# Kernel optimization log

Hardware: AMD Instinct MI355X
Metric: run time of the kernel (lower is better)

The kernel has to match this reference:

```python
import jax, jax.numpy as jnp
import numpy as np

N = 50000      # nodes
E = 800000     # directed edges (avg degree 16)
F_IN = 128     # dataset.num_features
H = 256        # hidden_channels
C = 40         # dataset.num_classes


def _glorot(k, shape):
    lim = float(np.sqrt(6.0 / (shape[0] + shape[1])))
    return jax.random.uniform(k, shape, jnp.float32, -lim, lim)


def setup_inputs() -> dict:
    key = jax.random.key(0)
    ks = jax.random.split(key, 8)
    x = jax.random.normal(ks[0], (N, F_IN), jnp.float32)
    edge_index = jax.random.randint(ks[1], (2, E), 0, N, dtype=jnp.int32)
    W1 = _glorot(ks[2], (F_IN, H));      b1 = jnp.zeros((H,), jnp.float32)
    W2 = _glorot(ks[3], (H, H // 2));    b2 = jnp.zeros((H // 2,), jnp.float32)
    W3 = _glorot(ks[4], (H // 2, H // 4)); b3 = jnp.zeros((H // 4,), jnp.float32)
    W4 = _glorot(ks[5], (H // 4, C));    b4 = jnp.zeros((C,), jnp.float32)
    return {"x": x, "edge_index": edge_index,
            "W1": W1, "b1": b1, "W2": W2, "b2": b2,
            "W3": W3, "b3": b3, "W4": W4, "b4": b4}


def reference(x, edge_index, W1, b1, W2, b2, W3, b3, W4, b4):
    # GCNConv with default add_self_loops=True and symmetric normalization.
    loops = jnp.arange(N, dtype=edge_index.dtype)
    src = jnp.concatenate([edge_index[0], loops])   # message sources
    dst = jnp.concatenate([edge_index[1], loops])   # aggregation targets
    # degree computed on target index (PyG default), incl. self-loops
    deg = jax.ops.segment_sum(jnp.ones_like(dst, jnp.float32), dst, num_segments=N)
    dinv = jnp.where(deg > 0, jax.lax.rsqrt(deg), 0.0)
    norm = dinv[src] * dinv[dst]                    # [E+N]

    def conv(h, W, b):
        h = h @ W                                   # transform first (PyG order)
        msg = h[src] * norm[:, None]                # gather + scale
        return jax.ops.segment_sum(msg, dst, num_segments=N) + b

    h = jax.nn.relu(conv(x, W1, b1))   # dropout = identity in eval mode
    h = jax.nn.relu(conv(h, W2, b2))
    h = jax.nn.relu(conv(h, W3, b3))
    return conv(h, W4, b4)
```

## Files before the change

kernel.cpp:

```cpp
#include <hip/hip_runtime.h>
#include <stdint.h>

#define NNODES 50000
#define NEDGES 800000
#define SCAN_NBLK ((NNODES + 255) / 256)
#define NB ((NNODES + 255) / 256)
#define EPB 4096
#define SCAT_NBLK ((NEDGES + EPB - 1) / EPB)

typedef __attribute__((ext_vector_type(8))) short bf16x8;
typedef __attribute__((ext_vector_type(4))) float f32x4;

__device__ inline unsigned short f2bf(float f) {
    unsigned u = __float_as_uint(f);
    return (unsigned short)((u + 0x7fffu + ((u >> 16) & 1u)) >> 16);
}
__device__ inline float bf2f(unsigned short h) {
    return __uint_as_float(((unsigned)h) << 16);
}


__global__ void zero_kernel(int* __restrict__ p, int n) {
    int i = blockIdx.x * blockDim.x + threadIdx.x;
    if (i < n) p[i] = 0;
}

__global__ __launch_bounds__(256) void bucket_count_kernel(const int* __restrict__ dst,
                                                           int* __restrict__ bhist) {
    __shared__ int h[NB];
    for (int b = threadIdx.x; b < NB; b += 256) h[b] = 0;
    __syncthreads();
    const int base = blockIdx.x * EPB;
#pragma unroll
    for (int i = 0; i < EPB / 256; ++i) {
        const int e = base + threadIdx.x + i * 256;
        if (e < NEDGES) atomicAdd(&h[dst[e] >> 8], 1);
    }
    __syncthreads();
    for (int b = threadIdx.x; b < NB; b += 256)
        if (h[b]) atomicAdd(&bhist[b], h[b]);
}

__global__ __launch_bounds__(256) void bucket_scan_kernel(const int* __restrict__ bhist,
                                                          int* __restrict__ bofs,
                                                          int* __restrict__ gcur) {
    __shared__ int s[256];
    const int t = threadIdx.x;
    s[t] = (t < NB) ? bhist[t] : 0;
    __syncthreads();
    for (int off = 1; off < 256; off <<= 1) {
        int v = (t >= off) ? s[t - off] : 0;
        __syncthreads();
        s[t] += v;
        __syncthreads();
    }
    if (t < NB) {
        const int excl = (t > 0) ? s[t - 1] : 0;
        bofs[t] = excl;
        gcur[t] = excl;
    }
    if (t == 255) bofs[NB] = s[255];
}

__global__ __launch_bounds__(256) void bucket_scatter_kernel(const int* __restrict__ src,
                                                             const int* __restrict__ dst,
                                                             int* __restrict__ gcur,
                                                             int2* __restrict__ gpair) {
    __shared__ int h[256];
    __shared__ int s[256];
    __shared__ int gof[256];
    __shared__ int2 pr[EPB];
    __shared__ int ga[EPB];

    const int t = threadIdx.x;
    const int base = blockIdx.x * EPB;
    const int nval = min(EPB, NEDGES - base);

    h[t] = 0;
    __syncthreads();
#pragma unroll
    for (int i = 0; i < EPB / 256; ++i) {
        const int e = base + t + i * 256;
        if (e < NEDGES) atomicAdd(&h[dst[e] >> 8], 1);
    }
    __syncthreads();
    s[t] = h[t];
    __syncthreads();
    for (int off = 1; off < 256; off <<= 1) {
        int v = (t >= off) ? s[t - off] : 0;
        __syncthreads();
        s[t] += v;
        __syncthreads();
    }
    {
        const int c = h[t];
        if (t < NB && c > 0) gof[t] = atomicAdd(&gcur[t], c);
        const int lofs = s[t] - c;
        h[t] = lofs;
        s[t] = lofs;
    }
    __syncthreads();
#pragma unroll
    for (int i = 0; i < EPB / 256; ++i) {
        const int e = base + t + i * 256;
        if (e < NEDGES) {
            const int d = dst[e];
            const int b = d >> 8;
            const int slot = atomicAdd(&h[b], 1);
            pr[slot] = make_int2(src[e], d);
            ga[slot] = gof[b] + (slot - s[b]);
        }
    }
    __syncthreads();
#pragma unroll
    for (int i = 0; i < EPB / 256; ++i) {
        const int slot = t + i * 256;
        if (slot < nval) gpair[ga[slot]] = pr[slot];
    }
}

__global__ __launch_bounds__(256) void deg_count_kernel(const int2* __restrict__ gpair,
                                                        const int* __restrict__ bofs,
                                                        int* __restrict__ cnt) {
    __shared__ int c[256];
    const int t = threadIdx.x;
    c[t] = 0;
    __syncthreads();
    const int beg = bofs[blockIdx.x], end = bofs[blockIdx.x + 1];
    for (int e = beg + t; e < end; e += 256) atomicAdd(&c[gpair[e].y & 255], 1);
    __syncthreads();
    const int node = blockIdx.x * 256 + t;
    if (node < NNODES) cnt[node] = c[t];
}

__global__ __launch_bounds__(256) void bucket_fill_kernel(const int2* __restrict__ gpair,
                                                          const int* __restrict__ bofs,
                                                          const int* __restrict__ rp,
                                                          int* __restrict__ col) {
    __shared__ int c[256];
    const int t = threadIdx.x;
    c[t] = 0;
    __syncthreads();
    const int beg = bofs[blockIdx.x], end = bofs[blockIdx.x + 1];
    for (int e = beg + t; e < end; e += 256) {
        const int2 p = gpair[e];
        const int r = atomicAdd(&c[p.y & 255], 1);
        col[rp[p.y] + r] = p.x;
    }
}


__global__ __launch_bounds__(256) void scan1_kernel(const int* __restrict__ cnt,
                                                    int* __restrict__ bsum) {
    const int i = blockIdx.x * 256 + threadIdx.x;
    int v = (i < NNODES) ? cnt[i] : 0;
#pragma unroll
    for (int off = 32; off > 0; off >>= 1) v += __shfl_down(v, off, 64);
    __shared__ int wsum[4];
    if ((threadIdx.x & 63) == 0) wsum[threadIdx.x >> 6] = v;
    __syncthreads();
    if (threadIdx.x == 0) bsum[blockIdx.x] = wsum[0] + wsum[1] + wsum[2] + wsum[3];
}

__global__ __launch_bounds__(256) void scan2_kernel(const int* __restrict__ bsum,
                                                    int* __restrict__ boff,
                                                    int* __restrict__ rp_last) {
    __shared__ int s[256];
    const int t = threadIdx.x;
    s[t] = (t < SCAN_NBLK) ? bsum[t] : 0;
    __syncthreads();
    for (int off = 1; off < 256; off <<= 1) {
        int v = (t >= off) ? s[t - off] : 0;
        __syncthreads();
        s[t] += v;
        __syncthreads();
    }
    if (t < SCAN_NBLK) boff[t] = (t > 0) ? s[t - 1] : 0;
    if (t == 255) rp_last[0] = s[255];
}

__global__ __launch_bounds__(256) void scan3_kernel(const int* __restrict__ cnt,
                                                    const int* __restrict__ boff,
                                                    int* __restrict__ rp,
                                                    float* __restrict__ dinv) {
    __shared__ int s[256];
    const int t = threadIdx.x;
    const int i = blockIdx.x * 256 + t;
    const int c = (i < NNODES) ? cnt[i] : 0;
    s[t] = c;
    __syncthreads();
    for (int off = 1; off < 256; off <<= 1) {
        int v = (t >= off) ? s[t - off] : 0;
        __syncthreads();
        s[t] += v;
        __syncthreads();
    }
    if (i < NNODES) {
        rp[i] = boff[blockIdx.x] + s[t] - c;
        dinv[i] = rsqrtf((float)(c + 1));
    }
}


__global__ __launch_bounds__(256) void cvt_kernel(const float* __restrict__ in,
                                                  unsigned short* __restrict__ out, int n4) {
    int i = blockIdx.x * 256 + threadIdx.x;
    if (i >= n4) return;
    float4 v = *(const float4*)(in + (size_t)i * 4);
    ushort4 h;
    h.x = f2bf(v.x); h.y = f2bf(v.y); h.z = f2bf(v.z); h.w = f2bf(v.w);
    *(ushort4*)(out + (size_t)i * 4) = h;
}


template <int VEC>
__device__ inline void vloadf(float (&d)[VEC], const float* __restrict__ p) {
    if constexpr (VEC == 2) { float2 t = *(const float2*)p; d[0]=t.x; d[1]=t.y; }
    else { d[0] = *p; }
}
template <int VEC>
__device__ inline void vloadbf(float (&d)[VEC], const unsigned short* __restrict__ p) {
    if constexpr (VEC == 2) {
        unsigned v = *(const unsigned*)p;
        d[0] = bf2f((unsigned short)(v & 0xffffu));
        d[1] = bf2f((unsigned short)(v >> 16));
    } else {
        d[0] = bf2f(*p);
    }
}
template <int VEC>
__device__ inline void vstoref(float* __restrict__ p, const float (&d)[VEC]) {
    if constexpr (VEC == 2) { *(float2*)p = make_float2(d[0], d[1]); }
    else { *p = d[0]; }
}

template <int F, int VEC, bool RELU, bool HAS_BIAS>
__global__ __launch_bounds__(256) void agg_kernel(const float* __restrict__ in32,
                                                  const unsigned short* __restrict__ inbf,
                                                  float* __restrict__ out,
                                                  const int* __restrict__ rp,
                                                  const int* __restrict__ colidx,
                                                  const float* __restrict__ dinv,
                                                  const float* __restrict__ bias) {
    const int wave = threadIdx.x >> 6;
    const int lane = threadIdx.x & 63;
    const int d = blockIdx.x * 4 + wave;
    if (d >= NNODES) return;
    constexpr int LANES = F / VEC;
    if (lane >= LANES) return;
    const int off = lane * VEC;

    const float dv = dinv[d];
    float acc[VEC];
    vloadf<VEC>(acc, in32 + (size_t)d * F + off);
#pragma unroll
    for (int v = 0; v < VEC; ++v) acc[v] *= dv;

    int j = rp[d];
    const int end = rp[d + 1];
    for (; j + 4 <= end; j += 4) {
        const int c0 = colidx[j + 0], c1 = colidx[j + 1], c2 = colidx[j + 2], c3 = colidx[j + 3];
        const float w0 = dinv[c0], w1 = dinv[c1], w2 = dinv[c2], w3 = dinv[c3];
        float t0[VEC], t1[VEC], t2[VEC], t3[VEC];
        vloadbf<VEC>(t0, inbf + (size_t)c0 * F + off);
        vloadbf<VEC>(t1, inbf + (size_t)c1 * F + off);
        vloadbf<VEC>(t2, inbf + (size_t)c2 * F + off);
        vloadbf<VEC>(t3, inbf + (size_t)c3 * F + off);
#pragma unroll
        for (int v = 0; v < VEC; ++v) acc[v] += w0 * t0[v] + w1 * t1[v] + w2 * t2[v] + w3 * t3[v];
    }
    for (; j < end; ++j) {
        const int c = colidx[j];
        const float wc = dinv[c];
        float t[VEC];
        vloadbf<VEC>(t, inbf + (size_t)c * F + off);
#pragma unroll
        for (int v = 0; v < VEC; ++v) acc[v] += wc * t[v];
    }

    float res[VEC];
#pragma unroll
    for (int v = 0; v < VEC; ++v) {
        float r = dv * acc[v];
        if constexpr (HAS_BIAS) r += bias[off + v];
        if constexpr (RELU) r = fmaxf(r, 0.0f);
        res[v] = r;
    }
    vstoref<VEC>(out + (size_t)d * F + off, res);
}


template <int K, int M>
__global__ __launch_bounds__(256) void repack_kernel(const float* __restrict__ W,
                                                     unsigned short* __restrict__ hi,
                                                     unsigned short* __restrict__ lo) {
    int i = blockIdx.x * 256 + threadIdx.x;
    if (i >= K * M) return;
    const int k = i / M, n = i % M;
    constexpr int KS = K / 32;
    const int cb = n >> 7;
    const int ct = (n >> 4) & 7;
    const int ln = ((k >> 3) & 3) * 16 + (n & 15);
    const int j  = k & 7;
    const int ks = k >> 5;
    const size_t o = ((((size_t)cb * KS + ks) * 8 + ct) * 64 + ln) * 8 + j;
    const float f = W[i];
    const unsigned short h = f2bf(f);
    hi[o] = h;
    lo[o] = f2bf(f - bf2f(h));
}


template <int K, int M, bool BIAS_RELU, bool WRITE_BF>
__global__ __launch_bounds__(256) void mfma_gemm_kernel(const float* __restrict__ A,
                                                        const unsigned short* __restrict__ Whi,
                                                        const unsigned short* __restrict__ Wlo,
                                                        const float* __restrict__ bias,
                                                        float* __restrict__ C,
                                                        unsigned short* __restrict__ Cbf) {
    constexpr int KS = K / 32;
    __shared__ char lds[32768];
    char* Ahi = lds;
    char* Alo = lds + 8192;
    char* Bhi = lds + 16384;
    char* Blo = lds + 24576;

    const int t = threadIdx.x;
    const int lane = t & 63;
    const int w = t >> 6;
    const int wr = w >> 1, wc = w & 1;
    const int r0 = blockIdx.x * 128;
    const int n0 = blockIdx.y * 128;

    const unsigned short* bhg = Whi + (size_t)blockIdx.y * KS * 4096;
    const unsigned short* blg = Wlo + (size_t)blockIdx.y * KS * 4096;

    f32x4 acc[4][4];
#pragma unroll
    for (int i = 0; i < 4; ++i)
#pragma unroll
        for (int j = 0; j < 4; ++j) acc[i][j] = (f32x4){0.f, 0.f, 0.f, 0.f};

    for (int ks = 0; ks < KS; ++ks) {
        const int k0 = ks * 32;

        {
            const char* gh = (const char*)(bhg + (size_t)ks * 4096);
            const char* gl = (const char*)(blg + (size_t)ks * 4096);
#pragma unroll
            for (int c = 0; c < 2; ++c) {
                const int ct = w * 2 + c;
                __builtin_amdgcn_global_load_lds(
                    (const __attribute__((address_space(1))) void*)(gh + ct * 1024 + lane * 16),
                    (__attribute__((address_space(3))) void*)(Bhi + ct * 1024), 16, 0, 0);
                __builtin_amdgcn_global_load_lds(
                    (const __attribute__((address_space(1))) void*)(gl + ct * 1024 + lane * 16),
                    (__attribute__((address_space(3))) void*)(Blo + ct * 1024), 16, 0, 0);
            }
        }

        float4 av[4];
#pragma unroll
        for (int i = 0; i < 4; ++i) {
            const int q = t + i * 256;
            const int row = q >> 3;
            const int kq = (q & 7) * 4;
            const int gr = r0 + row;
            float4 v = make_float4(0.f, 0.f, 0.f, 0.f);
            if (gr < NNODES) v = *(const float4*)(A + (size_t)gr * K + k0 + kq);
            av[i] = v;
        }
#pragma unroll
        for (int i = 0; i < 4; ++i) {
            const int q = t + i * 256;
            const int row = q >> 3;
            const int kq = (q & 7) * 4;
            const int rt = row >> 4, m = row & 15, quad = kq >> 3, j0 = kq & 7;
            const int off = rt * 1024 + (quad * 16 + m) * 16 + j0 * 2;
            const float4 v = av[i];
            ushort4 h, l;
            h.x = f2bf(v.x); l.x = f2bf(v.x - bf2f(h.x));
            h.y = f2bf(v.y); l.y = f2bf(v.y - bf2f(h.y));
            h.z = f2bf(v.z); l.z = f2bf(v.z - bf2f(h.z));
            h.w = f2bf(v.w); l.w = f2bf(v.w - bf2f(h.w));
            *(ushort4*)(Ahi + off) = h;
            *(ushort4*)(Alo + off) = l;
        }
        __syncthreads();

        bf16x8 ah[4], al[4], bh[4], bl[4];
#pragma unroll
        for (int i = 0; i < 4; ++i) {
            ah[i] = *(const bf16x8*)(Ahi + (wr * 4 + i) * 1024 + lane * 16);
            al[i] = *(const bf16x8*)(Alo + (wr * 4 + i) * 1024 + lane * 16);
            bh[i] = *(const bf16x8*)(Bhi + (wc * 4 + i) * 1024 + lane * 16);
            bl[i] = *(const bf16x8*)(Blo + (wc * 4 + i) * 1024 + lane * 16);
        }
#pragma unroll
        for (int i = 0; i < 4; ++i)
#pragma unroll
            for (int j = 0; j < 4; ++j) {
                acc[i][j] = __builtin_amdgcn_mfma_f32_16x16x32_bf16(ah[i], bh[j], acc[i][j], 0, 0, 0);
                acc[i][j] = __builtin_amdgcn_mfma_f32_16x16x32_bf16(ah[i], bl[j], acc[i][j], 0, 0, 0);
                acc[i][j] = __builtin_amdgcn_mfma_f32_16x16x32_bf16(al[i], bh[j], acc[i][j], 0, 0, 0);
            }
        __syncthreads();
    }

    const int quad = lane >> 4;
    const int cl = lane & 15;
#pragma unroll
    for (int i = 0; i < 4; ++i) {
#pragma unroll
        for (int j = 0; j < 4; ++j) {
            const int colg = n0 + wc * 64 + j * 16 + cl;
            float bv = 0.f;
            if constexpr (BIAS_RELU) bv = bias[colg];
#pragma unroll
            for (int r = 0; r < 4; ++r) {
                const int rowg = r0 + wr * 64 + i * 16 + quad * 4 + r;
                if (rowg < NNODES) {
                    float v = acc[i][j][r] + bv;
                    if constexpr (BIAS_RELU) v = fmaxf(v, 0.f);
                    C[(size_t)rowg * M + colg] = v;
                    if constexpr (WRITE_BF) Cbf[(size_t)rowg * M + colg] = f2bf(v);
                }
            }
        }
    }
}


template <int BM, int BN, int BK, int TM, int TN, bool BIAS_RELU, bool WRITE_BF>
__global__ __launch_bounds__(256) void gemm_kernel(const float* __restrict__ A,
                                                   const float* __restrict__ W,
                                                   const float* __restrict__ bias,
                                                   float* __restrict__ C,
                                                   unsigned short* __restrict__ Cbf,
                                                   int Nrows, int K, int M) {
    constexpr int TX = BN / TN;
    constexpr int TY = BM / TM;
    static_assert(TX * TY == 256, "thread grid must be 256");
    constexpr int A_LOADS = (BM * BK) / (256 * 4);
    constexpr int W_LOADS = (BN * BK) / (256 * 4);
    static_assert(A_LOADS >= 1 && W_LOADS >= 1, "tile too small");

    const int tid = threadIdx.x;
    const int tx = tid % TX;
    const int ty = tid / TX;
    const int r0 = blockIdx.x * BM;
    const int c0 = blockIdx.y * BN;

    __shared__ float As[BK][BM + 4];
    __shared__ float Ws[BK][BN];

    float acc[TM][TN] = {};

    for (int k0 = 0; k0 < K; k0 += BK) {
#pragma unroll
        for (int l = 0; l < A_LOADS; ++l) {
            const int idx = tid + l * 256;
            const int row = idx / (BK / 4);
            const int kq = idx % (BK / 4);
            float4 v = make_float4(0.f, 0.f, 0.f, 0.f);
            const int gr = r0 + row;
            if (gr < Nrows) v = *(const float4*)(A + (size_t)gr * K + k0 + kq * 4);
            As[kq * 4 + 0][row] = v.x;
            As[kq * 4 + 1][row] = v.y;
            As[kq * 4 + 2][row] = v.z;
            As[kq * 4 + 3][row] = v.w;
        }
#pragma unroll
        for (int l = 0; l < W_LOADS; ++l) {
            const int idx = tid + l * 256;
            const int kk = idx / (BN / 4);
            const int cq = idx % (BN / 4);
            const int gc = c0 + cq * 4;
            float4 v;
            const float* wrow = W + (size_t)(k0 + kk) * M;
            if (gc + 3 < M) {
                v = *(const float4*)(wrow + gc);
            } else {
                v.x = (gc + 0 < M) ? wrow[gc + 0] : 0.f;
                v.y = (gc + 1 < M) ? wrow[gc + 1] : 0.f;
                v.z = (gc + 2 < M) ? wrow[gc + 2] : 0.f;
                v.w = (gc + 3 < M) ? wrow[gc + 3] : 0.f;
            }
            *(float4*)&Ws[kk][cq * 4] = v;
        }
        __syncthreads();

#pragma unroll
        for (int kk = 0; kk < BK; ++kk) {
            float a[TM], b[TN];
#pragma unroll
            for (int i = 0; i < TM; ++i) a[i] = As[kk][ty * TM + i];
#pragma unroll
            for (int j = 0; j < TN; ++j) b[j] = Ws[kk][tx * TN + j];
#pragma unroll
            for (int i = 0; i < TM; ++i)
#pragma unroll
                for (int j = 0; j < TN; ++j) acc[i][j] += a[i] * b[j];
        }
        __syncthreads();
    }

#pragma unroll
    for (int i = 0; i < TM; ++i) {
        const int gr = r0 + ty * TM + i;
        if (gr >= Nrows) continue;
#pragma unroll
        for (int j = 0; j < TN; ++j) {
            const int gc = c0 + tx * TN + j;
            if (gc >= M) continue;
            float v = acc[i][j];
            if constexpr (BIAS_RELU) v = fmaxf(v + bias[gc], 0.0f);
            C[(size_t)gr * M + gc] = v;
            if constexpr (WRITE_BF) Cbf[(size_t)gr * M + gc] = f2bf(v);
        }
    }
}


extern "C" void kernel_launch(void* const* d_in, const int* in_sizes, int n_in,
                              void* d_out, int out_size, void* d_ws, size_t ws_size,
                              hipStream_t stream) {
    const float* x  = (const float*)d_in[0];
    const int* ei   = (const int*)d_in[1];
    const float* W1 = (const float*)d_in[2];
    const float* b1 = (const float*)d_in[3];
    const float* W2 = (const float*)d_in[4];
    const float* b2 = (const float*)d_in[5];
    const float* W3 = (const float*)d_in[6];
    const float* b3 = (const float*)d_in[7];
    const float* W4 = (const float*)d_in[8];
    const float* b4 = (const float*)d_in[9];
    float* out = (float*)d_out;
    const int* esrc = ei;
    const int* edst = ei + NEDGES;

    char* w = (char*)d_ws;
    auto alloc = [&](size_t bytes) -> void* {
        void* p = (void*)w;
        w += (bytes + 255) & ~(size_t)255;
        return p;
    };
    int* cnt    = (int*)alloc((size_t)NNODES * 4);
    int* rp     = (int*)alloc((size_t)(NNODES + 1) * 4);
    int* col    = (int*)alloc((size_t)NEDGES * 4);
    float* dinv = (float*)alloc((size_t)NNODES * 4);
    int* bsum   = (int*)alloc((size_t)SCAN_NBLK * 4);
    int* boff   = (int*)alloc((size_t)SCAN_NBLK * 4);
    int* bhist  = (int*)alloc((size_t)NB * 4);
    int* bofs   = (int*)alloc((size_t)(NB + 1) * 4);
    int* gcur   = (int*)alloc((size_t)NB * 4);
    int2* gpair = (int2*)alloc((size_t)NEDGES * 8);
    unsigned short* W1hi = (unsigned short*)alloc((size_t)128 * 256 * 2);
    unsigned short* W1lo = (unsigned short*)alloc((size_t)128 * 256 * 2);
    unsigned short* W2hi = (unsigned short*)alloc((size_t)256 * 128 * 2);
    unsigned short* W2lo = (unsigned short*)alloc((size_t)256 * 128 * 2);
    float* B0   = (float*)alloc((size_t)NNODES * 256 * 4);
    float* B1   = (float*)alloc((size_t)NNODES * 128 * 4);
    float* B2   = (float*)alloc((size_t)NNODES * 128 * 4);
    unsigned short* xbf  = (unsigned short*)alloc((size_t)NNODES * 128 * 2);
    unsigned short* B1bf = (unsigned short*)alloc((size_t)NNODES * 128 * 2);
    unsigned short* B0bf = (unsigned short*)alloc((size_t)NNODES * 64 * 2);

    repack_kernel<128, 256><<<(128 * 256 + 255) / 256, 256, 0, stream>>>(W1, W1hi, W1lo);
    repack_kernel<256, 128><<<(256 * 128 + 255) / 256, 256, 0, stream>>>(W2, W2hi, W2lo);
    cvt_kernel<<<(NNODES * 128 / 4 + 255) / 256, 256, 0, stream>>>(x, xbf, NNODES * 128 / 4);

    zero_kernel<<<1, 256, 0, stream>>>(bhist, NB);
    bucket_count_kernel<<<SCAT_NBLK, 256, 0, stream>>>(edst, bhist);
    bucket_scan_kernel<<<1, 256, 0, stream>>>(bhist, bofs, gcur);
    bucket_scatter_kernel<<<SCAT_NBLK, 256, 0, stream>>>(esrc, edst, gcur, gpair);
    deg_count_kernel<<<NB, 256, 0, stream>>>(gpair, bofs, cnt);
    scan1_kernel<<<SCAN_NBLK, 256, 0, stream>>>(cnt, bsum);
    scan2_kernel<<<1, 256, 0, stream>>>(bsum, boff, rp + NNODES);
    scan3_kernel<<<SCAN_NBLK, 256, 0, stream>>>(cnt, boff, rp, dinv);
    bucket_fill_kernel<<<NB, 256, 0, stream>>>(gpair, bofs, rp, col);

    const int aggGrid = (NNODES + 3) / 4;
    const int rowBlks = (NNODES + 127) / 128;

    agg_kernel<128, 2, false, false><<<aggGrid, 256, 0, stream>>>(x, xbf, B2, rp, col, dinv, nullptr);
    mfma_gemm_kernel<128, 256, true, false>
        <<<dim3(rowBlks, 2), 256, 0, stream>>>(B2, W1hi, W1lo, b1, B0, nullptr);

    mfma_gemm_kernel<256, 128, false, true>
        <<<dim3(rowBlks, 1), 256, 0, stream>>>(B0, W2hi, W2lo, nullptr, B1, B1bf);
    agg_kernel<128, 2, true, true><<<aggGrid, 256, 0, stream>>>(B1, B1bf, B2, rp, col, dinv, b2);

    gemm_kernel<64, 64, 16, 4, 4, false, true>
        <<<dim3((NNODES + 63) / 64, 1), 256, 0, stream>>>(B2, W3, nullptr, B0, B0bf, NNODES, 128, 64);
    agg_kernel<64, 1, true, true><<<aggGrid, 256, 0, stream>>>(B0, B0bf, B1, rp, col, dinv, b3);

    gemm_kernel<64, 64, 16, 4, 4, false, true>
        <<<dim3((NNODES + 63) / 64, 1), 256, 0, stream>>>(B1, W4, nullptr, B0, B0bf, NNODES, 64, 40);
    agg_kernel<40, 1, false, true><<<aggGrid, 256, 0, stream>>>(B0, B0bf, out, rp, col, dinv, b4);
}
```

Baseline: 383.7 us.

## Fuse CSR build into one per-bucket kernel and shrink MFMA GEMM row tile

Result: faster. 365.9 us (-4.6%).

```diff
diff --git a/kernel.cpp b/kernel.cpp
--- a/kernel.cpp
+++ b/kernel.cpp
@@ -3,7 +3,6 @@
 
 #define NNODES 50000
 #define NEDGES 800000
-#define SCAN_NBLK ((NNODES + 255) / 256)
 #define NB ((NNODES + 255) / 256)
 #define EPB 4096
 #define SCAT_NBLK ((NEDGES + EPB - 1) / EPB)
@@ -43,7 +42,8 @@
 
 __global__ __launch_bounds__(256) void bucket_scan_kernel(const int* __restrict__ bhist,
                                                           int* __restrict__ bofs,
-                                                          int* __restrict__ gcur) {
+                                                          int* __restrict__ gcur,
+                                                          int* __restrict__ rp_last) {
     __shared__ int s[256];
     const int t = threadIdx.x;
     s[t] = (t < NB) ? bhist[t] : 0;
@@ -59,17 +59,17 @@
         bofs[t] = excl;
         gcur[t] = excl;
     }
-    if (t == 255) bofs[NB] = s[255];
+    if (t == 255) { bofs[NB] = s[255]; rp_last[0] = s[255]; }
 }
 
 __global__ __launch_bounds__(256) void bucket_scatter_kernel(const int* __restrict__ src,
                                                              const int* __restrict__ dst,
                                                              int* __restrict__ gcur,
-                                                             int2* __restrict__ gpair) {
+                                                             unsigned* __restrict__ gpk) {
     __shared__ int h[256];
     __shared__ int s[256];
     __shared__ int gof[256];
-    __shared__ int2 pr[EPB];
+    __shared__ unsigned pr[EPB];
     __shared__ int ga[EPB];
 
     const int t = threadIdx.x;
@@ -107,7 +107,7 @@
             const int d = dst[e];
             const int b = d >> 8;
             const int slot = atomicAdd(&h[b], 1);
-            pr[slot] = make_int2(src[e], d);
+            pr[slot] = ((unsigned)(d & 255) << 16) | (unsigned)src[e];
             ga[slot] = gof[b] + (slot - s[b]);
         }
     }
@@ -115,59 +115,26 @@
 #pragma unroll
     for (int i = 0; i < EPB / 256; ++i) {
         const int slot = t + i * 256;
-        if (slot < nval) gpair[ga[slot]] = pr[slot];
-    }
-}
-
-__global__ __launch_bounds__(256) void deg_count_kernel(const int2* __restrict__ gpair,
-                                                        const int* __restrict__ bofs,
-                                                        int* __restrict__ cnt) {
+        if (slot < nval) gpk[ga[slot]] = pr[slot];
+    }
+}
+
+__global__ __launch_bounds__(256) void csr_fill_kernel(const unsigned* __restrict__ gpk,
+                                                       const int* __restrict__ bofs,
+                                                       int* __restrict__ rp,
+                                                       float* __restrict__ dinv,
+                                                       int* __restrict__ col) {
     __shared__ int c[256];
+    __shared__ int s[256];
+    __shared__ int cur[256];
     const int t = threadIdx.x;
+    const int b = blockIdx.x;
+    const int beg = bofs[b], end = bofs[b + 1];
     c[t] = 0;
     __syncthreads();
-    const int beg = bofs[blockIdx.x], end = bofs[blockIdx.x + 1];
-    for (int e = beg + t; e < end; e += 256) atomicAdd(&c[gpair[e].y & 255], 1);
-    __syncthreads();
-    const int node = blockIdx.x * 256 + t;
-    if (node < NNODES) cnt[node] = c[t];
-}
-
-__global__ __launch_bounds__(256) void bucket_fill_kernel(const int2* __restrict__ gpair,
-                                                          const int* __restrict__ bofs,
-                                                          const int* __restrict__ rp,
-                                                          int* __restrict__ col) {
-    __shared__ int c[256];
-    const int t = threadIdx.x;
-    c[t] = 0;
-    __syncthreads();
-    const int beg = bofs[blockIdx.x], end = bofs[blockIdx.x + 1];
-    for (int e = beg + t; e < end; e += 256) {
-        const int2 p = gpair[e];
-        const int r = atomicAdd(&c[p.y & 255], 1);
-        col[rp[p.y] + r] = p.x;
-    }
-}
-
-
-__global__ __launch_bounds__(256) void scan1_kernel(const int* __restrict__ cnt,
-                                                    int* __restrict__ bsum) {
-    const int i = blockIdx.x * 256 + threadIdx.x;
-    int v = (i < NNODES) ? cnt[i] : 0;
-#pragma unroll
-    for (int off = 32; off > 0; off >>= 1) v += __shfl_down(v, off, 64);
-    __shared__ int wsum[4];
-    if ((threadIdx.x & 63) == 0) wsum[threadIdx.x >> 6] = v;
-    __syncthreads();
-    if (threadIdx.x == 0) bsum[blockIdx.x] = wsum[0] + wsum[1] + wsum[2] + wsum[3];
-}
-
-__global__ __launch_bounds__(256) void scan2_kernel(const int* __restrict__ bsum,
-                                                    int* __restrict__ boff,
-                                                    int* __restrict__ rp_last) {
-    __shared__ int s[256];
-    const int t = threadIdx.x;
-    s[t] = (t < SCAN_NBLK) ? bsum[t] : 0;
+    for (int e = beg + t; e < end; e += 256) atomicAdd(&c[gpk[e] >> 16], 1);
+    __syncthreads();
+    s[t] = c[t];
     __syncthreads();
     for (int off = 1; off < 256; off <<= 1) {
         int v = (t >= off) ? s[t - off] : 0;
@@ -175,29 +142,18 @@
         s[t] += v;
         __syncthreads();
     }
-    if (t < SCAN_NBLK) boff[t] = (t > 0) ? s[t - 1] : 0;
-    if (t == 255) rp_last[0] = s[255];
-}
-
-__global__ __launch_bounds__(256) void scan3_kernel(const int* __restrict__ cnt,
-                                                    const int* __restrict__ boff,
-                                                    int* __restrict__ rp,
-                                                    float* __restrict__ dinv) {
-    __shared__ int s[256];
-    const int t = threadIdx.x;
-    const int i = blockIdx.x * 256 + t;
-    const int c = (i < NNODES) ? cnt[i] : 0;
-    s[t] = c;
-    __syncthreads();
-    for (int off = 1; off < 256; off <<= 1) {
-        int v = (t >= off) ? s[t - off] : 0;
-        __syncthreads();
-        s[t] += v;
-        __syncthreads();
-    }
-    if (i < NNODES) {
-        rp[i] = boff[blockIdx.x] + s[t] - c;
-        dinv[i] = rsqrtf((float)(c + 1));
+    const int excl = s[t] - c[t];
+    cur[t] = excl;
+    const int node = b * 256 + t;
+    if (node < NNODES) {
+        rp[node] = beg + excl;
+        dinv[node] = rsqrtf((float)(c[t] + 1));
+    }
+    __syncthreads();
+    for (int e = beg + t; e < end; e += 256) {
+        const unsigned p = gpk[e];
+        const int r = atomicAdd(&cur[p >> 16], 1);
+        col[beg + r] = (int)(p & 0xffffu);
     }
 }
 
@@ -311,7 +267,7 @@
 }
 
 
-template <int K, int M, bool BIAS_RELU, bool WRITE_BF>
+template <int K, int M, int BM, bool BIAS_RELU, bool WRITE_BF>
 __global__ __launch_bounds__(256) void mfma_gemm_kernel(const float* __restrict__ A,
                                                         const unsigned short* __restrict__ Whi,
                                                         const unsigned short* __restrict__ Wlo,
@@ -319,27 +275,30 @@
                                                         float* __restrict__ C,
                                                         unsigned short* __restrict__ Cbf) {
     constexpr int KS = K / 32;
-    __shared__ char lds[32768];
+    constexpr int ASZ = BM * 64;
+    constexpr int CI = (BM == 128) ? 4 : 2;
+    __shared__ char lds[2 * ASZ + 16384];
     char* Ahi = lds;
-    char* Alo = lds + 8192;
-    char* Bhi = lds + 16384;
-    char* Blo = lds + 24576;
+    char* Alo = lds + ASZ;
+    char* Bhi = lds + 2 * ASZ;
+    char* Blo = lds + 2 * ASZ + 8192;
 
     const int t = threadIdx.x;
     const int lane = t & 63;
     const int w = t >> 6;
-    const int wr = w >> 1, wc = w & 1;
-    const int r0 = blockIdx.x * 128;
+    const int wr = (BM == 128) ? (w >> 1) : 0;
+    const int wc = (BM == 128) ? (w & 1) : w;
+    const int r0 = blockIdx.x * BM;
     const int n0 = blockIdx.y * 128;
 
     const unsigned short* bhg = Whi + (size_t)blockIdx.y * KS * 4096;
     const unsigned short* blg = Wlo + (size_t)blockIdx.y * KS * 4096;
 
-    f32x4 acc[4][4];
+    f32x4 acc[4][CI];
 #pragma unroll
     for (int i = 0; i < 4; ++i)
 #pragma unroll
-        for (int j = 0; j < 4; ++j) acc[i][j] = (f32x4){0.f, 0.f, 0.f, 0.f};
+        for (int j = 0; j < CI; ++j) acc[i][j] = (f32x4){0.f, 0.f, 0.f, 0.f};
 
     for (int ks = 0; ks < KS; ++ks) {
         const int k0 = ks * 32;
@@ -359,9 +318,9 @@
             }
         }
 
-        float4 av[4];
-#pragma unroll
-        for (int i = 0; i < 4; ++i) {
+        float4 av[BM / 32];
+#pragma unroll
+        for (int i = 0; i < BM / 32; ++i) {
             const int q = t + i * 256;
             const int row = q >> 3;
             const int kq = (q & 7) * 4;
@@ -371,7 +330,7 @@
             av[i] = v;
         }
 #pragma unroll
-        for (int i = 0; i < 4; ++i) {
+        for (int i = 0; i < BM / 32; ++i) {
             const int q = t + i * 256;
             const int row = q >> 3;
             const int kq = (q & 7) * 4;
@@ -388,18 +347,21 @@
         }
         __syncthreads();
 
-        bf16x8 ah[4], al[4], bh[4], bl[4];
+        bf16x8 ah[4], al[4], bh[CI], bl[CI];
 #pragma unroll
         for (int i = 0; i < 4; ++i) {
             ah[i] = *(const bf16x8*)(Ahi + (wr * 4 + i) * 1024 + lane * 16);
             al[i] = *(const bf16x8*)(Alo + (wr * 4 + i) * 1024 + lane * 16);
-            bh[i] = *(const bf16x8*)(Bhi + (wc * 4 + i) * 1024 + lane * 16);
-            bl[i] = *(const bf16x8*)(Blo + (wc * 4 + i) * 1024 + lane * 16);
+        }
+#pragma unroll
+        for (int j = 0; j < CI; ++j) {
+            bh[j] = *(const bf16x8*)(Bhi + (wc * CI + j) * 1024 + lane * 16);
+            bl[j] = *(const bf16x8*)(Blo + (wc * CI + j) * 1024 + lane * 16);
         }
 #pragma unroll
         for (int i = 0; i < 4; ++i)
 #pragma unroll
-            for (int j = 0; j < 4; ++j) {
+            for (int j = 0; j < CI; ++j) {
                 acc[i][j] = __builtin_amdgcn_mfma_f32_16x16x32_bf16(ah[i], bh[j], acc[i][j], 0, 0, 0);
                 acc[i][j] = __builtin_amdgcn_mfma_f32_16x16x32_bf16(ah[i], bl[j], acc[i][j], 0, 0, 0);
                 acc[i][j] = __builtin_amdgcn_mfma_f32_16x16x32_bf16(al[i], bh[j], acc[i][j], 0, 0, 0);
@@ -412,8 +374,8 @@
 #pragma unroll
     for (int i = 0; i < 4; ++i) {
 #pragma unroll
-        for (int j = 0; j < 4; ++j) {
-            const int colg = n0 + wc * 64 + j * 16 + cl;
+        for (int j = 0; j < CI; ++j) {
+            const int colg = n0 + wc * (CI * 16) + j * 16 + cl;
             float bv = 0.f;
             if constexpr (BIAS_RELU) bv = bias[colg];
 #pragma unroll
@@ -545,16 +507,13 @@
         w += (bytes + 255) & ~(size_t)255;
         return p;
     };
-    int* cnt    = (int*)alloc((size_t)NNODES * 4);
     int* rp     = (int*)alloc((size_t)(NNODES + 1) * 4);
     int* col    = (int*)alloc((size_t)NEDGES * 4);
     float* dinv = (float*)alloc((size_t)NNODES * 4);
-    int* bsum   = (int*)alloc((size_t)SCAN_NBLK * 4);
-    int* boff   = (int*)alloc((size_t)SCAN_NBLK * 4);
     int* bhist  = (int*)alloc((size_t)NB * 4);
     int* bofs   = (int*)alloc((size_t)(NB + 1) * 4);
     int* gcur   = (int*)alloc((size_t)NB * 4);
-    int2* gpair = (int2*)alloc((size_t)NEDGES * 8);
+    unsigned* gpk = (unsigned*)alloc((size_t)NEDGES * 4);
     unsigned short* W1hi = (unsigned short*)alloc((size_t)128 * 256 * 2);
     unsigned short* W1lo = (unsigned short*)alloc((size_t)128 * 256 * 2);
     unsigned short* W2hi = (unsigned short*)alloc((size_t)256 * 128 * 2);
@@ -572,30 +531,26 @@
 
     zero_kernel<<<1, 256, 0, stream>>>(bhist, NB);
     bucket_count_kernel<<<SCAT_NBLK, 256, 0, stream>>>(edst, bhist);
-    bucket_scan_kernel<<<1, 256, 0, stream>>>(bhist, bofs, gcur);
-    bucket_scatter_kernel<<<SCAT_NBLK, 256, 0, stream>>>(esrc, edst, gcur, gpair);
-    deg_count_kernel<<<NB, 256, 0, stream>>>(gpair, bofs, cnt);
-    scan1_kernel<<<SCAN_NBLK, 256, 0, stream>>>(cnt, bsum);
-    scan2_kernel<<<1, 256, 0, stream>>>(bsum, boff, rp + NNODES);
-    scan3_kernel<<<SCAN_NBLK, 256, 0, stream>>>(cnt, boff, rp, dinv);
-    bucket_fill_kernel<<<NB, 256, 0, stream>>>(gpair, bofs, rp, col);
+    bucket_scan_kernel<<<1, 256, 0, stream>>>(bhist, bofs, gcur, rp + NNODES);
+    bucket_scatter_kernel<<<SCAT_NBLK, 256, 0, stream>>>(esrc, edst, gcur, gpk);
+    csr_fill_kernel<<<NB, 256, 0, stream>>>(gpk, bofs, rp, dinv, col);
 
     const int aggGrid = (NNODES + 3) / 4;
-    const int rowBlks = (NNODES + 127) / 128;
+    const int rowBlks64 = (NNODES + 63) / 64;
 
     agg_kernel<128, 2, false, false><<<aggGrid, 256, 0, stream>>>(x, xbf, B2, rp, col, dinv, nullptr);
-    mfma_gemm_kernel<128, 256, true, false>
-        <<<dim3(rowBlks, 2), 256, 0, stream>>>(B2, W1hi, W1lo, b1, B0, nullptr);
-
-    mfma_gemm_kernel<256, 128, false, true>
-        <<<dim3(rowBlks, 1), 256, 0, stream>>>(B0, W2hi, W2lo, nullptr, B1, B1bf);
+    mfma_gemm_kernel<128, 256, 64, true, false>
+        <<<dim3(rowBlks64, 2), 256, 0, stream>>>(B2, W1hi, W1lo, b1, B0, nullptr);
+
+    mfma_gemm_kernel<256, 128, 64, false, true>
+        <<<dim3(rowBlks64, 1), 256, 0, stream>>>(B0, W2hi, W2lo, nullptr, B1, B1bf);
     agg_kernel<128, 2, true, true><<<aggGrid, 256, 0, stream>>>(B1, B1bf, B2, rp, col, dinv, b2);
 
     gemm_kernel<64, 64, 16, 4, 4, false, true>
-        <<<dim3((NNODES + 63) / 64, 1), 256, 0, stream>>>(B2, W3, nullptr, B0, B0bf, NNODES, 128, 64);
+        <<<dim3(rowBlks64, 1), 256, 0, stream>>>(B2, W3, nullptr, B0, B0bf, NNODES, 128, 64);
     agg_kernel<64, 1, true, true><<<aggGrid, 256, 0, stream>>>(B0, B0bf, B1, rp, col, dinv, b3);
 
     gemm_kernel<64, 64, 16, 4, 4, false, true>
-        <<<dim3((NNODES + 63) / 64, 1), 256, 0, stream>>>(B1, W4, nullptr, B0, B0bf, NNODES, 64, 40);
+        <<<dim3(rowBlks64, 1), 256, 0, stream>>>(B1, W4, nullptr, B0, B0bf, NNODES, 64, 40);
     agg_kernel<40, 1, false, true><<<aggGrid, 256, 0, stream>>>(B0, B0bf, out, rp, col, dinv, b4);
 }
```
